# Kernel tuning notes

Hardware: AMD Instinct MI355X
Metric: run time of the kernel (lower is better)

## Reference

```python
import jax, jax.numpy as jnp
import numpy as np

B, N, D = 32, 128, 1024


def _euclid_cost(a, b):
    # a: [N, D], b: [N, D] -> [N, N] Euclidean distances (torch.cdist p=2)
    a = a.astype(np.float64)
    b = b.astype(np.float64)
    sq = (a * a).sum(-1)[:, None] + (b * b).sum(-1)[None, :] - 2.0 * (a @ b.T)
    return np.sqrt(np.maximum(sq, 0.0))


def _hungarian(cost):
    """Exact LAP via shortest augmenting path (Kuhn-Munkres with potentials).
    Returns col_for_row: row i is matched to column col_for_row[i].
    Equivalent to scipy.optimize.linear_sum_assignment on a square matrix
    (row_ind == arange(N))."""
    n = cost.shape[0]
    INF = 1e18
    c = cost.astype(np.float64)
    u = np.zeros(n + 1)
    v = np.zeros(n + 1)
    p = np.zeros(n + 1, dtype=np.int64)   # p[j] = row matched to column j (1-based)
    way = np.zeros(n + 1, dtype=np.int64)
    for i in range(1, n + 1):
        p[0] = i
        j0 = 0
        minv = np.full(n + 1, INF)
        used = np.zeros(n + 1, dtype=bool)
        while True:
            used[j0] = True
            i0 = p[j0]
            free = ~used[1:]
            cand = c[i0 - 1] - u[i0] - v[1:]
            better = free & (cand < minv[1:])
            idx = np.nonzero(better)[0]
            minv[idx + 1] = cand[idx]
            way[idx + 1] = j0
            free_j = np.nonzero(free)[0] + 1
            j1 = free_j[np.argmin(minv[free_j])]
            delta = minv[j1]
            u[p[used]] += delta
            v[used] -= delta
            minv[~used] -= delta
            j0 = j1
            if p[j0] == 0:
                break
        while j0:
            j1 = way[j0]
            p[j0] = p[j1]
            j0 = j1
    col_for_row = np.zeros(n, dtype=np.int64)
    for j in range(1, n + 1):
        col_for_row[p[j] - 1] = j - 1
    return col_for_row


def _match(pred_nodes, target_nodes):
    # Host-side exact bipartite matching (mirrors the .cpu() + scipy solve;
    # non-differentiable, indices treated as constants like torch's detach()).
    pn = np.asarray(jax.device_get(pred_nodes))
    tn = np.asarray(jax.device_get(target_nodes))
    cols = [_hungarian(_euclid_cost(pn[b], tn[b])) for b in range(pn.shape[0])]
    return jnp.asarray(np.stack(cols))  # [B, N] int64


def setup_inputs() -> dict:
    key = jax.random.key(0)
    k1, k2, k3, k4 = jax.random.split(key, 4)
    return {
        "pred_nodes": jax.random.normal(k1, (B, N, D), dtype=jnp.float32),
        "target_nodes": jax.random.normal(k2, (B, N, D), dtype=jnp.float32),
        "pred_adj": jax.random.normal(k3, (B, N, N), dtype=jnp.float32),
        "target_adj": jax.random.normal(k4, (B, N, N), dtype=jnp.float32),
    }


def reference(pred_nodes, target_nodes, pred_adj, target_adj):
    col = _match(pred_nodes, target_nodes)  # [B, N]; row_ind is identity
    # matched target nodes: target_nodes[b][col_ind]
    tn_m = jnp.take_along_axis(target_nodes, col[:, :, None], axis=1)  # [B, N, D]
    # nn.MSELoss() = mean over elements per sample; losses summed over batch
    node_loss = jnp.mean((pred_nodes - tn_m) ** 2, axis=(1, 2)).sum()
    # target_adj[b][col_ind][:, col_ind]; pred_adj row_ind gather is identity
    ta_m = jnp.take_along_axis(target_adj, col[:, :, None], axis=1)
    ta_m = jnp.take_along_axis(ta_m, col[:, None, :], axis=2)  # [B, N, N]
    edge_loss = jnp.mean((pred_adj - ta_m) ** 2, axis=(1, 2)).sum()
    return node_loss, edge_loss
```

## Files before the change

### kernel.cpp

```cpp
#include <hip/hip_runtime.h>
#include <hip/hip_bf16.h>
#include <math.h>

#define BB 32
#define NN 128
#define DD 1024
#define INF64 1e30

__global__ __launch_bounds__(64) void cost_kernel(const float* __restrict__ pred,
                                                  const float* __restrict__ tgt,
                                                  double* __restrict__ cost) {
  __shared__ float a_s[8 * DD];
  __shared__ double red_s[64];
  __shared__ double na_s[8];
  int blk = blockIdx.x;
  int b = blk >> 4;
  int it = (blk & 15) << 3;
  const float* Ab = pred + ((size_t)b * NN + it) * DD;
  const float* Bb = tgt + (size_t)b * NN * DD;
  const int lane = threadIdx.x;
  for (int t = lane; t < 8 * DD / 4; t += 64) {
    ((float4*)a_s)[t] = ((const float4*)Ab)[t];
  }
  __syncthreads();
  {
    int r = lane >> 3, o = lane & 7;
    const float* ar = a_s + (size_t)r * DD;
    double s = 0.0;
    for (int k = o; k < DD; k += 8) { double x = (double)ar[k]; s += x * x; }
    red_s[lane] = s;
  }
  __syncthreads();
  if (lane < 8) {
    double s = 0.0;
#pragma unroll
    for (int m = 0; m < 8; m++) s += red_s[lane * 8 + m];
    na_s[lane] = s;
  }
  __syncthreads();
  const float4* brow0 = (const float4*)(Bb + (size_t)lane * DD);
  const float4* brow1 = (const float4*)(Bb + (size_t)(lane + 64) * DD);
  double acc0[8], acc1[8];
#pragma unroll
  for (int r = 0; r < 8; r++) { acc0[r] = 0.0; acc1[r] = 0.0; }
  double nb0 = 0.0, nb1 = 0.0;
  for (int k4 = 0; k4 < DD / 4; k4++) {
    float4 b0 = brow0[k4];
    float4 b1 = brow1[k4];
    double d00 = (double)b0.x, d01 = (double)b0.y, d02 = (double)b0.z, d03 = (double)b0.w;
    double d10 = (double)b1.x, d11 = (double)b1.y, d12 = (double)b1.z, d13 = (double)b1.w;
    nb0 += d00 * d00 + d01 * d01 + d02 * d02 + d03 * d03;
    nb1 += d10 * d10 + d11 * d11 + d12 * d12 + d13 * d13;
#pragma unroll
    for (int r = 0; r < 8; r++) {
      float4 av = ((const float4*)(a_s + (size_t)r * DD))[k4];
      double a0 = (double)av.x, a1 = (double)av.y, a2 = (double)av.z, a3 = (double)av.w;
      acc0[r] += a0 * d00 + a1 * d01 + a2 * d02 + a3 * d03;
      acc1[r] += a0 * d10 + a1 * d11 + a2 * d12 + a3 * d13;
    }
  }
#pragma unroll
  for (int r = 0; r < 8; r++) {
    double sq0 = na_s[r] + nb0 - 2.0 * acc0[r];
    double sq1 = na_s[r] + nb1 - 2.0 * acc1[r];
    size_t base = (((size_t)b * NN) + it + r) * NN;
    cost[base + lane] = sqrt(fmax(sq0, 0.0));
    cost[base + lane + 64] = sqrt(fmax(sq1, 0.0));
  }
}

union f64u { double d; unsigned int i[2]; };

__device__ __forceinline__ double readlane_f64(double x, int lane) {
  f64u u; u.d = x;
  f64u v;
  v.i[0] = (unsigned)__builtin_amdgcn_readlane((int)u.i[0], lane);
  v.i[1] = (unsigned)__builtin_amdgcn_readlane((int)u.i[1], lane);
  return v.d;
}

__device__ __forceinline__ double readpair_f64(double a, double b, int idx) {
  int l = (idx - 1) & 63;
  double ra = readlane_f64(a, l);
  double rb = readlane_f64(b, l);
  return ((idx - 1) >> 6) ? rb : ra;
}

__device__ __forceinline__ int readpair_i32(int a, int b, int idx) {
  int l = (idx - 1) & 63;
  int ra = __builtin_amdgcn_readlane(a, l);
  int rb = __builtin_amdgcn_readlane(b, l);
  return ((idx - 1) >> 6) ? rb : ra;
}

__device__ __forceinline__ double pack_key(double m, int idx) {
  unsigned long long bits = __double_as_longlong(fmax(m, 0.0));
  bits = (bits & ~127ull) | (unsigned long long)idx;
  return __longlong_as_double(bits);
}

#define DPP_MIN_STEP(r, CTRL)                                                        \
  do {                                                                               \
    f64u _t; _t.d = (r);                                                             \
    f64u _s;                                                                         \
    _s.i[0] = (unsigned)__builtin_amdgcn_update_dpp((int)_t.i[0], (int)_t.i[0],      \
                                                    (CTRL), 0xF, 0xF, false);        \
    _s.i[1] = (unsigned)__builtin_amdgcn_update_dpp((int)_t.i[1], (int)_t.i[1],      \
                                                    (CTRL), 0xF, 0xF, false);        \
    (r) = fmin((r), _s.d);                                                           \
  } while (0)

#define DPP_MIN_CHAIN(r)          \
  do {                            \
    DPP_MIN_STEP(r, 0x111);       \
    DPP_MIN_STEP(r, 0x112);       \
    DPP_MIN_STEP(r, 0x114);       \
    DPP_MIN_STEP(r, 0x118);       \
    DPP_MIN_STEP(r, 0x142);       \
    DPP_MIN_STEP(r, 0x143);       \
  } while (0)

__global__ __launch_bounds__(64) void hungarian_kernel(const double* __restrict__ cost,
                                                       int* __restrict__ colfor) {
  extern __shared__ double lds[];
  const int b = blockIdx.x;
  const double* C = cost + (size_t)b * NN * NN;
  const int lane = threadIdx.x;
  const int jA = lane + 1;
  const int jB = lane + 65;

  {
    const double2* src = (const double2*)C;
    double2* dst = (double2*)lds;
#pragma unroll 8
    for (int t = lane; t < NN * NN / 2; t += 64) dst[t] = src[t];
  }
  __syncthreads();

  double vA = INF64, vB = INF64;
  int argA = 0, argB = 0;
#pragma unroll 4
  for (int i = 0; i < NN; i++) {
    double cA = lds[(size_t)i * NN + lane];
    double cB = lds[(size_t)i * NN + lane + 64];
    if (cA < vA) { vA = cA; argA = i + 1; }
    if (cB < vB) { vB = cB; argB = i + 1; }
  }

  unsigned long long asgLo = 0ull, asgHi = 0ull;
  int pA = 0, pB = 0;
  for (int j = 1; j <= NN; j++) {
    int ar = readpair_i32(argA, argB, j);
    bool freeRow = (ar <= 64) ? !((asgLo >> (ar - 1)) & 1ull)
                              : !((asgHi >> (ar - 65)) & 1ull);
    if (freeRow) {
      if (ar <= 64) asgLo |= 1ull << (ar - 1); else asgHi |= 1ull << (ar - 65);
      if (j == jA) pA = ar;
      if (j == jB) pB = ar;
    }
  }

  unsigned long long freeLo = __ballot(pA == 0);
  unsigned long long freeHi = __ballot(pB == 0);

  double uA = 0.0, uB = 0.0;
  unsigned long long mLo = ~asgLo, mHi = ~asgHi;

  while ((mLo | mHi) != 0ull) {
    int i = mLo ? (__builtin_ctzll(mLo) + 1) : (__builtin_ctzll(mHi) + 65);
    if (i <= 64) mLo &= ~(1ull << (i - 1)); else mHi &= ~(1ull << (i - 65));

    double minvA = INF64, minvB = INF64;
    int wayA = 0, wayB = 0;
    int usedA = 0, usedB = 0;
    unsigned long long usedRowLo = 0ull, usedRowHi = 0ull;
    int j0 = 0;
    int i0 = i;
    double cA = lds[(size_t)(i0 - 1) * NN + lane];
    double cB = lds[(size_t)(i0 - 1) * NN + lane + 64];
    double u_i0 = readpair_f64(uA, uB, i0);
    while (true) {
      usedA |= (j0 == jA);
      usedB |= (j0 == jB);
      if (i0 <= 64) usedRowLo |= 1ull << (i0 - 1); else usedRowHi |= 1ull << (i0 - 65);
      double candA = cA - u_i0 - vA;
      double candB = cB - u_i0 - vB;
      if (!usedA && candA < minvA) { minvA = candA; wayA = j0; }
      if (!usedB && candB < minvB) { minvB = candB; wayB = j0; }
      double kA = pack_key(usedA ? INF64 : minvA, lane);
      double kB = pack_key(usedB ? INF64 : minvB, lane + 64);
      double r = fmin(kA, kB);
      DPP_MIN_CHAIN(r);
      double rmin = readlane_f64(r, 63);
      unsigned long long bits = __double_as_longlong(rmin);
      int j1 = (int)(bits & 127ull) + 1;
      double delta = __longlong_as_double((long long)(bits & ~127ull));
      bool isFree = (j1 <= 64) ? ((freeLo >> (j1 - 1)) & 1ull)
                               : ((freeHi >> (j1 - 65)) & 1ull);
      int i0next = 0;
      double ncA = 0.0, ncB = 0.0, nu = 0.0;
      if (!isFree) {
        i0next = readpair_i32(pA, pB, j1);
        ncA = lds[(size_t)(i0next - 1) * NN + lane];
        ncB = lds[(size_t)(i0next - 1) * NN + lane + 64];
        nu = readpair_f64(uA, uB, i0next);
      }
      if ((usedRowLo >> lane) & 1ull) uA += delta;
      if ((usedRowHi >> lane) & 1ull) uB += delta;
      if (usedA) vA -= delta; else minvA -= delta;
      if (usedB) vB -= delta; else minvB -= delta;
      j0 = j1;
      if (isFree) break;
      i0 = i0next; cA = ncA; cB = ncB; u_i0 = nu;
    }
    int jfin = j0;
    int j = jfin;
    while (j) {
      int wj = readpair_i32(wayA, wayB, j);
      int pn = (wj == 0) ? i : readpair_i32(pA, pB, wj);
      if (j == jA) pA = pn;
      if (j == jB) pB = pn;
      j = wj;
    }
    if (jfin <= 64) freeLo &= ~(1ull << (jfin - 1));
    else            freeHi &= ~(1ull << (jfin - 65));
  }
  colfor[b * NN + (pA - 1)] = jA - 1;
  colfor[b * NN + (pB - 1)] = jB - 1;
}

__global__ __launch_bounds__(256) void node_loss_kernel(const float* __restrict__ pred,
                                                        const float* __restrict__ tgt,
                                                        const int* __restrict__ col,
                                                        double* __restrict__ partial) {
  const size_t total = (size_t)BB * NN * (DD / 4);
  double s = 0.0;
  for (size_t idx = (size_t)blockIdx.x * blockDim.x + threadIdx.x; idx < total;
       idx += (size_t)gridDim.x * blockDim.x) {
    size_t k4 = idx & (DD / 4 - 1);
    size_t bi = idx / (DD / 4);
    int i = (int)(bi & (NN - 1));
    int b = (int)(bi >> 7);
    int c = col[b * NN + i];
    float4 pv = ((const float4*)pred)[idx];
    float4 tv = ((const float4*)(tgt + ((size_t)b * NN + c) * DD))[k4];
    float d0 = pv.x - tv.x, d1 = pv.y - tv.y, d2 = pv.z - tv.z, d3 = pv.w - tv.w;
    s += (double)d0 * d0 + (double)d1 * d1 + (double)d2 * d2 + (double)d3 * d3;
  }
  __shared__ double red[256];
  red[threadIdx.x] = s;
  __syncthreads();
  for (int off = 128; off > 0; off >>= 1) {
    if (threadIdx.x < off) red[threadIdx.x] += red[threadIdx.x + off];
    __syncthreads();
  }
  if (threadIdx.x == 0) partial[blockIdx.x] = red[0];
}

__global__ __launch_bounds__(256) void edge_loss_kernel(const float* __restrict__ padj,
                                                        const float* __restrict__ tadj,
                                                        const int* __restrict__ col,
                                                        double* __restrict__ partial) {
  const size_t total = (size_t)BB * NN * NN;
  double s = 0.0;
  for (size_t idx = (size_t)blockIdx.x * blockDim.x + threadIdx.x; idx < total;
       idx += (size_t)gridDim.x * blockDim.x) {
    int j = (int)(idx & (NN - 1));
    size_t bi = idx >> 7;
    int i = (int)(bi & (NN - 1));
    int b = (int)(bi >> 7);
    int ci = col[b * NN + i];
    int cj = col[b * NN + j];
    float diff = padj[idx] - tadj[((size_t)b * NN + ci) * NN + cj];
    s += (double)diff * (double)diff;
  }
  __shared__ double red[256];
  red[threadIdx.x] = s;
  __syncthreads();
  for (int off = 128; off > 0; off >>= 1) {
    if (threadIdx.x < off) red[threadIdx.x] += red[threadIdx.x + off];
    __syncthreads();
  }
  if (threadIdx.x == 0) partial[blockIdx.x] = red[0];
}

__global__ __launch_bounds__(256) void finalize_kernel(const double* __restrict__ nodeP, int nNode,
                                                       const double* __restrict__ edgeP, int nEdge,
                                                       float* __restrict__ out) {
  __shared__ double red[256];
  double s = 0.0;
  for (int t = threadIdx.x; t < nNode; t += 256) s += nodeP[t];
  red[threadIdx.x] = s;
  __syncthreads();
  for (int off = 128; off > 0; off >>= 1) {
    if (threadIdx.x < off) red[threadIdx.x] += red[threadIdx.x + off];
    __syncthreads();
  }
  double nodeSum = red[0];
  __syncthreads();
  s = 0.0;
  for (int t = threadIdx.x; t < nEdge; t += 256) s += edgeP[t];
  red[threadIdx.x] = s;
  __syncthreads();
  for (int off = 128; off > 0; off >>= 1) {
    if (threadIdx.x < off) red[threadIdx.x] += red[threadIdx.x + off];
    __syncthreads();
  }
  if (threadIdx.x == 0) {
    out[0] = (float)(nodeSum / (double)(NN * DD));
    out[1] = (float)(red[0] / (double)(NN * NN));
  }
}

extern "C" void kernel_launch(void* const* d_in, const int* in_sizes, int n_in,
                              void* d_out, int out_size, void* d_ws, size_t ws_size,
                              hipStream_t stream) {
  const float* pred_nodes   = (const float*)d_in[0];
  const float* target_nodes = (const float*)d_in[1];
  const float* pred_adj     = (const float*)d_in[2];
  const float* target_adj   = (const float*)d_in[3];
  float* out = (float*)d_out;

  char* ws = (char*)d_ws;
  double* cost = (double*)ws;
  size_t off = (size_t)BB * NN * NN * sizeof(double);
  int* col = (int*)(ws + off);
  off += (size_t)BB * NN * sizeof(int);
  double* nodeP = (double*)(ws + off);
  double* edgeP = nodeP + 512;

  cost_kernel<<<BB * 16, 64, 0, stream>>>(pred_nodes, target_nodes, cost);
  hungarian_kernel<<<BB, 64, 131072, stream>>>(cost, col);
  node_loss_kernel<<<512, 256, 0, stream>>>(pred_nodes, target_nodes, col, nodeP);
  edge_loss_kernel<<<128, 256, 0, stream>>>(pred_adj, target_adj, col, edgeP);
  finalize_kernel<<<1, 256, 0, stream>>>(nodeP, 512, edgeP, 128, out);
}
```

Measured before the change: 940.5 us.

## Store A tile as doubles in LDS, remap cost blocks, simplify Hungarian loop

The cost kernel now converts the pred tile to double once when loading it into dynamic shared memory (64 KB), so the inner loop no longer converts floats each iteration. Block indices are remapped so that neighbouring blocks handle different batches. The Hungarian kernel drops the free-column bitmasks and the prefetch of the next row, and instead checks p[j1]==0 and loads the cost row inside the loop. The larger LDS footprint lowers occupancy, and the serial Hungarian loop loses its prefetch overlap.

New measurement: 810.7 us. 1.16x faster.

```diff
diff --git a/kernel.cpp b/kernel.cpp
--- a/kernel.cpp
+++ b/kernel.cpp
@@ -10,32 +10,39 @@
 __global__ __launch_bounds__(64) void cost_kernel(const float* __restrict__ pred,
                                                   const float* __restrict__ tgt,
                                                   double* __restrict__ cost) {
-  __shared__ float a_s[8 * DD];
+  extern __shared__ double a_s[];
   __shared__ double red_s[64];
   __shared__ double na_s[8];
-  int blk = blockIdx.x;
-  int b = blk >> 4;
-  int it = (blk & 15) << 3;
+  int s = blockIdx.x;
+  int r8 = s & 7;
+  int m = s >> 3;
+  int t = m & 15;
+  int q = m >> 4;
+  int b = 8 * q + r8;
+  int it = t << 3;
   const float* Ab = pred + ((size_t)b * NN + it) * DD;
   const float* Bb = tgt + (size_t)b * NN * DD;
   const int lane = threadIdx.x;
-  for (int t = lane; t < 8 * DD / 4; t += 64) {
-    ((float4*)a_s)[t] = ((const float4*)Ab)[t];
+  for (int tdx = lane; tdx < 8 * DD / 4; tdx += 64) {
+    float4 v = ((const float4*)Ab)[tdx];
+    double2* d = (double2*)&a_s[(size_t)tdx * 4];
+    d[0] = double2{(double)v.x, (double)v.y};
+    d[1] = double2{(double)v.z, (double)v.w};
   }
   __syncthreads();
   {
     int r = lane >> 3, o = lane & 7;
-    const float* ar = a_s + (size_t)r * DD;
-    double s = 0.0;
-    for (int k = o; k < DD; k += 8) { double x = (double)ar[k]; s += x * x; }
-    red_s[lane] = s;
+    const double* ar = a_s + (size_t)r * DD;
+    double sum = 0.0;
+    for (int k = o; k < DD; k += 8) { double x = ar[k]; sum += x * x; }
+    red_s[lane] = sum;
   }
   __syncthreads();
   if (lane < 8) {
-    double s = 0.0;
+    double sum = 0.0;
 #pragma unroll
-    for (int m = 0; m < 8; m++) s += red_s[lane * 8 + m];
-    na_s[lane] = s;
+    for (int mm = 0; mm < 8; mm++) sum += red_s[lane * 8 + mm];
+    na_s[lane] = sum;
   }
   __syncthreads();
   const float4* brow0 = (const float4*)(Bb + (size_t)lane * DD);
@@ -53,10 +60,11 @@
     nb1 += d10 * d10 + d11 * d11 + d12 * d12 + d13 * d13;
 #pragma unroll
     for (int r = 0; r < 8; r++) {
-      float4 av = ((const float4*)(a_s + (size_t)r * DD))[k4];
-      double a0 = (double)av.x, a1 = (double)av.y, a2 = (double)av.z, a3 = (double)av.w;
-      acc0[r] += a0 * d00 + a1 * d01 + a2 * d02 + a3 * d03;
-      acc1[r] += a0 * d10 + a1 * d11 + a2 * d12 + a3 * d13;
+      const double2* ap = (const double2*)(a_s + (size_t)r * DD + (size_t)k4 * 4);
+      double2 x = ap[0];
+      double2 y = ap[1];
+      acc0[r] += x.x * d00 + x.y * d01 + y.x * d02 + y.y * d03;
+      acc1[r] += x.x * d10 + x.y * d11 + y.x * d12 + y.y * d13;
     }
   }
 #pragma unroll
@@ -160,15 +168,12 @@
     }
   }
 
-  unsigned long long freeLo = __ballot(pA == 0);
-  unsigned long long freeHi = __ballot(pB == 0);
-
   double uA = 0.0, uB = 0.0;
-  unsigned long long mLo = ~asgLo, mHi = ~asgHi;
-
-  while ((mLo | mHi) != 0ull) {
-    int i = mLo ? (__builtin_ctzll(mLo) + 1) : (__builtin_ctzll(mHi) + 65);
-    if (i <= 64) mLo &= ~(1ull << (i - 1)); else mHi &= ~(1ull << (i - 65));
+
+  for (int i = 1; i <= NN; i++) {
+    bool seeded = (i <= 64) ? ((asgLo >> (i - 1)) & 1ull)
+                            : ((asgHi >> (i - 65)) & 1ull);
+    if (seeded) continue;
 
     double minvA = INF64, minvB = INF64;
     int wayA = 0, wayB = 0;
@@ -176,13 +181,15 @@
     unsigned long long usedRowLo = 0ull, usedRowHi = 0ull;
     int j0 = 0;
     int i0 = i;
-    double cA = lds[(size_t)(i0 - 1) * NN + lane];
-    double cB = lds[(size_t)(i0 - 1) * NN + lane + 64];
-    double u_i0 = readpair_f64(uA, uB, i0);
+    int jfin;
     while (true) {
       usedA |= (j0 == jA);
       usedB |= (j0 == jB);
       if (i0 <= 64) usedRowLo |= 1ull << (i0 - 1); else usedRowHi |= 1ull << (i0 - 65);
+      double u_i0 = readpair_f64(uA, uB, i0);
+      const double* crow = lds + (size_t)(i0 - 1) * NN;
+      double cA = crow[lane];
+      double cB = crow[lane + 64];
       double candA = cA - u_i0 - vA;
       double candB = cB - u_i0 - vB;
       if (!usedA && candA < minvA) { minvA = candA; wayA = j0; }
@@ -195,25 +202,15 @@
       unsigned long long bits = __double_as_longlong(rmin);
       int j1 = (int)(bits & 127ull) + 1;
       double delta = __longlong_as_double((long long)(bits & ~127ull));
-      bool isFree = (j1 <= 64) ? ((freeLo >> (j1 - 1)) & 1ull)
-                               : ((freeHi >> (j1 - 65)) & 1ull);
-      int i0next = 0;
-      double ncA = 0.0, ncB = 0.0, nu = 0.0;
-      if (!isFree) {
-        i0next = readpair_i32(pA, pB, j1);
-        ncA = lds[(size_t)(i0next - 1) * NN + lane];
-        ncB = lds[(size_t)(i0next - 1) * NN + lane + 64];
-        nu = readpair_f64(uA, uB, i0next);
-      }
       if ((usedRowLo >> lane) & 1ull) uA += delta;
       if ((usedRowHi >> lane) & 1ull) uB += delta;
       if (usedA) vA -= delta; else minvA -= delta;
       if (usedB) vB -= delta; else minvB -= delta;
+      int pj1 = readpair_i32(pA, pB, j1);
       j0 = j1;
-      if (isFree) break;
-      i0 = i0next; cA = ncA; cB = ncB; u_i0 = nu;
+      if (pj1 == 0) { jfin = j1; break; }
+      i0 = pj1;
     }
-    int jfin = j0;
     int j = jfin;
     while (j) {
       int wj = readpair_i32(wayA, wayB, j);
@@ -222,8 +219,6 @@
       if (j == jB) pB = pn;
       j = wj;
     }
-    if (jfin <= 64) freeLo &= ~(1ull << (jfin - 1));
-    else            freeHi &= ~(1ull << (jfin - 65));
   }
   colfor[b * NN + (pA - 1)] = jA - 1;
   colfor[b * NN + (pB - 1)] = jB - 1;
@@ -329,7 +324,7 @@
   double* nodeP = (double*)(ws + off);
   double* edgeP = nodeP + 512;
 
-  cost_kernel<<<BB * 16, 64, 0, stream>>>(pred_nodes, target_nodes, cost);
+  cost_kernel<<<BB * 16, 64, 65536, stream>>>(pred_nodes, target_nodes, cost);
   hungarian_kernel<<<BB, 64, 131072, stream>>>(cost, col);
   node_loss_kernel<<<512, 256, 0, stream>>>(pred_nodes, target_nodes, col, nodeP);
   edge_loss_kernel<<<128, 256, 0, stream>>>(pred_adj, target_adj, col, edgeP);
```
